# Kernel tuning notes

Measured on AMD Instinct MI355X. Metric: run time of the kernel, lower is better.

Reference implementation:

```python
import jax, jax.numpy as jnp
import numpy as np

N_NODES = 200000
N_SUPER = 20000
N_EDGES = 640000
EMB = 256


def setup_inputs() -> dict:
    key = jax.random.key(0)
    ks = jax.random.split(key, 8)
    x = jax.random.normal(ks[0], (N_NODES, EMB), dtype=jnp.float32)
    new_supernode_x = jax.random.normal(ks[1], (N_SUPER, EMB), dtype=jnp.float32)
    supernode_edge_index = jax.random.randint(ks[2], (2, N_EDGES), 0, N_NODES, dtype=jnp.int64)
    # supernode indices must be unique (torch `x[idx] += v` assumes no duplicate writes)
    supernode_idx = jnp.arange(N_SUPER, dtype=jnp.int64)
    graph_batch = jax.random.randint(ks[3], (N_NODES,), 0, 1024, dtype=jnp.int64)  # unused by forward
    s = 1.0 / np.sqrt(EMB)  # torch.nn.Linear default init scale
    W1 = jax.random.uniform(ks[4], (EMB, EMB), minval=-s, maxval=s, dtype=jnp.float32)
    b1 = jax.random.uniform(ks[5], (EMB,), minval=-s, maxval=s, dtype=jnp.float32)
    W2 = jax.random.uniform(ks[6], (EMB, EMB), minval=-s, maxval=s, dtype=jnp.float32)
    b2 = jax.random.uniform(ks[7], (EMB,), minval=-s, maxval=s, dtype=jnp.float32)
    return {
        "x": x,
        "new_supernode_x": new_supernode_x,
        "supernode_edge_index": supernode_edge_index,
        "supernode_idx": supernode_idx,
        "graph_batch": graph_batch,
        "W1": W1,
        "b1": b1,
        "W2": W2,
        "b2": b2,
    }


def reference(x, new_supernode_x, supernode_edge_index, supernode_idx, graph_batch, W1, b1, W2, b2):
    # step 1: project metagraph supernode embeddings, add into bg-graph rows at supernode_idx
    sn_proj = new_supernode_x @ W1.T + b1                 # [S, D]
    x1 = x.at[supernode_idx].add(sn_proj)                 # [N, D]
    # step 2: gather src rows (AFTER step-1 update), project, scatter-add to dst rows
    src = supernode_edge_index[1]
    dst = supernode_edge_index[0]
    msg = x1[src] @ W2.T + b2                             # [E, D]
    return x1.at[dst].add(msg)                            # [N, D]
```

## Files before the change

kernel.cpp:

```cpp
#include <hip/hip_runtime.h>

#define N_NODES 200000
#define N_SUPER 20000
#define N_EDGES 640000
#define EMB 256

typedef unsigned short ushort_t;
typedef unsigned short ushort8 __attribute__((ext_vector_type(8)));

static __device__ __forceinline__ ushort_t f2bf(float f) {
    unsigned int b = __float_as_uint(f);
    unsigned int r = (b + 0x7FFFu + ((b >> 16) & 1u)) >> 16;
    return (ushort_t)r;
}

__global__ __launch_bounds__(256) void copy_f4(const float4* __restrict__ s,
                                               float4* __restrict__ d, int n) {
    int i = blockIdx.x * 256 + threadIdx.x;
    if (i < n) d[i] = s[i];
}

__global__ __launch_bounds__(256) void hist_dst(const int* __restrict__ ei,
                                                int* __restrict__ counts) {
    int e = blockIdx.x * 256 + threadIdx.x;
    if (e < N_EDGES) atomicAdd(&counts[ei[e]], 1);
}

__global__ __launch_bounds__(256) void block_sums(const int* __restrict__ counts,
                                                  int* __restrict__ partials, int N) {
    __shared__ int sh[256];
    int tid = threadIdx.x;
    int i = blockIdx.x * 256 + tid;
    sh[tid] = (i < N) ? counts[i] : 0;
    __syncthreads();
    for (int off = 128; off > 0; off >>= 1) {
        if (tid < off) sh[tid] += sh[tid + off];
        __syncthreads();
    }
    if (tid == 0) partials[blockIdx.x] = sh[0];
}

__global__ __launch_bounds__(256) void scan_partials(int* __restrict__ partials, int NB) {
    __shared__ int sh[256];
    int tid = threadIdx.x;
    int carry = 0;
    for (int c0 = 0; c0 < NB; c0 += 256) {
        int i = c0 + tid;
        int v = (i < NB) ? partials[i] : 0;
        sh[tid] = v;
        __syncthreads();
        for (int off = 1; off < 256; off <<= 1) {
            int t = (tid >= off) ? sh[tid - off] : 0;
            __syncthreads();
            sh[tid] += t;
            __syncthreads();
        }
        int incl = sh[tid];
        int total = sh[255];
        if (i < NB) partials[i] = carry + incl - v;
        carry += total;
        __syncthreads();
    }
}

__global__ __launch_bounds__(256) void scan_blocks(const int* __restrict__ counts,
                                                   const int* __restrict__ partials,
                                                   int* __restrict__ base, int N) {
    __shared__ int sh[256];
    int tid = threadIdx.x;
    int b = blockIdx.x;
    int i = b * 256 + tid;
    int c = (i < N) ? counts[i] : 0;
    sh[tid] = c;
    __syncthreads();
    for (int off = 1; off < 256; off <<= 1) {
        int t = (tid >= off) ? sh[tid - off] : 0;
        __syncthreads();
        sh[tid] += t;
        __syncthreads();
    }
    if (i < N) base[i] = partials[b] + sh[tid] - c;
    if (i == N - 1) base[N] = partials[b] + sh[tid];
}

__global__ __launch_bounds__(256) void fill_bucket(const int* __restrict__ ei,
                                                   const int* __restrict__ base,
                                                   int* __restrict__ cursor,
                                                   int* __restrict__ bucket) {
    int e = blockIdx.x * 256 + threadIdx.x;
    if (e >= N_EDGES) return;
    int d = ei[e];
    int s = ei[N_EDGES + e];
    int pos = atomicAdd(&cursor[d], 1);
    bucket[base[d] + pos] = s;
}

__global__ __launch_bounds__(256) void gather_sum(const int* __restrict__ bucket,
                                                  const int* __restrict__ base,
                                                  const float* __restrict__ x1,
                                                  ushort_t* __restrict__ agg) {
    int node = blockIdx.x * 4 + (threadIdx.x >> 6);
    int lane = threadIdx.x & 63;
    if (node >= N_NODES) return;
    int j0 = base[node], j1 = base[node + 1];
    float4 acc = make_float4(0.f, 0.f, 0.f, 0.f);
    for (int j = j0; j < j1; ++j) {
        int s = bucket[j];
        float4 v = *(const float4*)(x1 + (size_t)s * EMB + lane * 4);
        acc.x += v.x; acc.y += v.y; acc.z += v.z; acc.w += v.w;
    }
    ushort4 p;
    p.x = f2bf(acc.x); p.y = f2bf(acc.y); p.z = f2bf(acc.z); p.w = f2bf(acc.w);
    *(ushort4*)(agg + (size_t)node * EMB + lane * 4) = p;
}

template <bool A_BF16>
__global__ __launch_bounds__(256) void gemm_add(
    const void* __restrict__ Ap, const float* __restrict__ W,
    const float* __restrict__ bias, const int* __restrict__ deg,
    const int* __restrict__ idx, float* __restrict__ out, int M) {
    __shared__ float At[64][68];
    __shared__ float Wt[64][68];
    const int row0 = blockIdx.x * 64;
    const int col0 = blockIdx.y * 64;
    const int tid = threadIdx.x;
    const int tr = tid >> 4, tc = tid & 15;
    float acc[4][4] = {};

    for (int k0 = 0; k0 < EMB; k0 += 64) {
        __syncthreads();
        if constexpr (A_BF16) {
            const ushort_t* A = (const ushort_t*)Ap;
            for (int t = tid; t < 512; t += 256) {
                int r = t >> 3, kq = t & 7;
                int m = row0 + r;
                float vals[8] = {0, 0, 0, 0, 0, 0, 0, 0};
                if (m < M) {
                    ushort8 u = *(const ushort8*)(A + (size_t)m * EMB + k0 + kq * 8);
                    #pragma unroll
                    for (int j = 0; j < 8; ++j)
                        vals[j] = __uint_as_float((unsigned int)u[j] << 16);
                }
                #pragma unroll
                for (int j = 0; j < 8; ++j) At[kq * 8 + j][r] = vals[j];
            }
        } else {
            const float* A = (const float*)Ap;
            for (int t = tid; t < 1024; t += 256) {
                int r = t >> 4, kq = t & 15;
                int m = row0 + r;
                float4 v = make_float4(0.f, 0.f, 0.f, 0.f);
                if (m < M) v = *(const float4*)(A + (size_t)m * EMB + k0 + kq * 4);
                At[kq * 4 + 0][r] = v.x; At[kq * 4 + 1][r] = v.y;
                At[kq * 4 + 2][r] = v.z; At[kq * 4 + 3][r] = v.w;
            }
        }
        for (int t = tid; t < 1024; t += 256) {
            int r = t >> 4, kq = t & 15;
            float4 w = *(const float4*)(W + (size_t)(col0 + r) * EMB + k0 + kq * 4);
            Wt[kq * 4 + 0][r] = w.x; Wt[kq * 4 + 1][r] = w.y;
            Wt[kq * 4 + 2][r] = w.z; Wt[kq * 4 + 3][r] = w.w;
        }
        __syncthreads();
        #pragma unroll 8
        for (int k = 0; k < 64; ++k) {
            float4 a = *(const float4*)&At[k][tr * 4];
            float4 w = *(const float4*)&Wt[k][tc * 4];
            float av[4] = {a.x, a.y, a.z, a.w};
            float wv[4] = {w.x, w.y, w.z, w.w};
            #pragma unroll
            for (int i = 0; i < 4; ++i)
                #pragma unroll
                for (int j = 0; j < 4; ++j)
                    acc[i][j] += av[i] * wv[j];
        }
    }

    #pragma unroll
    for (int i = 0; i < 4; ++i) {
        int m = row0 + tr * 4 + i;
        if (m >= M) continue;
        int orow = idx ? idx[m] : m;
        float coef = deg ? (float)deg[m] : 1.0f;
        float* op = out + (size_t)orow * EMB + col0 + tc * 4;
        #pragma unroll
        for (int j = 0; j < 4; ++j)
            op[j] += acc[i][j] + bias[col0 + tc * 4 + j] * coef;
    }
}

extern "C" void kernel_launch(void* const* d_in, const int* in_sizes, int n_in,
                              void* d_out, int out_size, void* d_ws, size_t ws_size,
                              hipStream_t stream) {
    const float* x    = (const float*)d_in[0];
    const float* snx  = (const float*)d_in[1];
    const int*   ei   = (const int*)d_in[2];
    const int*   sidx = (const int*)d_in[3];
    const float* W1   = (const float*)d_in[5];
    const float* b1   = (const float*)d_in[6];
    const float* W2   = (const float*)d_in[7];
    const float* b2   = (const float*)d_in[8];
    float* out = (float*)d_out;

    ushort_t* agg  = (ushort_t*)d_ws;
    int* counts    = (int*)(agg + (size_t)N_NODES * EMB);
    int* cursor    = counts + N_NODES;
    int* base      = cursor + N_NODES;
    int* bucket    = base + (N_NODES + 1);
    int* partials  = bucket + N_EDGES;

    const int NB = (N_NODES + 255) / 256;

    hipMemsetAsync(counts, 0, 2 * N_NODES * sizeof(int), stream);

    int n4 = N_NODES * EMB / 4;
    copy_f4<<<(n4 + 255) / 256, 256, 0, stream>>>((const float4*)x, (float4*)out, n4);

    dim3 g1((N_SUPER + 63) / 64, EMB / 64);
    gemm_add<false><<<g1, 256, 0, stream>>>(snx, W1, b1, nullptr, sidx, out, N_SUPER);

    hist_dst<<<(N_EDGES + 255) / 256, 256, 0, stream>>>(ei, counts);
    block_sums<<<NB, 256, 0, stream>>>(counts, partials, N_NODES);
    scan_partials<<<1, 256, 0, stream>>>(partials, NB);
    scan_blocks<<<NB, 256, 0, stream>>>(counts, partials, base, N_NODES);
    fill_bucket<<<(N_EDGES + 255) / 256, 256, 0, stream>>>(ei, base, cursor, bucket);

    gather_sum<<<(N_NODES + 3) / 4, 256, 0, stream>>>(bucket, base, out, agg);

    dim3 g2((N_NODES + 63) / 64, EMB / 64);
    gemm_add<true><<<g2, 256, 0, stream>>>(agg, W2, b2, counts, nullptr, out, N_NODES);
}
```

Baseline: 1.029 ms.

## Replace FP32 SIMT GEMMs with split-bf16 MFMA kernels holding weights in registers

Both projection GEMMs now run on bf16 MFMA instructions instead of scalar FP32 FMAs through shared memory. W is split into high and low bf16 parts so accuracy stays close to FP32, and the FP32 A input is split the same way for the W1 GEMM. Each 512-thread block keeps all of W in registers across a persistent loop over 16-row tiles, so there is no shared-memory staging and no syncthreads. The cost is extra MFMA passes for the split and heavy register use. The tile math also assumes M is a multiple of 16, with no row bounds check.

```diff
diff --git a/kernel.cpp b/kernel.cpp
--- a/kernel.cpp
+++ b/kernel.cpp
@@ -6,7 +6,8 @@
 #define EMB 256
 
 typedef unsigned short ushort_t;
-typedef unsigned short ushort8 __attribute__((ext_vector_type(8)));
+typedef __attribute__((ext_vector_type(8))) short bf16x8;
+typedef __attribute__((ext_vector_type(4))) float f32x4;
 
 static __device__ __forceinline__ ushort_t f2bf(float f) {
     unsigned int b = __float_as_uint(f);
@@ -115,77 +116,91 @@
 }
 
 template <bool A_BF16>
-__global__ __launch_bounds__(256) void gemm_add(
+__global__ __launch_bounds__(512) void gemm_mfma(
     const void* __restrict__ Ap, const float* __restrict__ W,
     const float* __restrict__ bias, const int* __restrict__ deg,
-    const int* __restrict__ idx, float* __restrict__ out, int M) {
-    __shared__ float At[64][68];
-    __shared__ float Wt[64][68];
-    const int row0 = blockIdx.x * 64;
-    const int col0 = blockIdx.y * 64;
-    const int tid = threadIdx.x;
-    const int tr = tid >> 4, tc = tid & 15;
-    float acc[4][4] = {};
-
-    for (int k0 = 0; k0 < EMB; k0 += 64) {
-        __syncthreads();
+    const int* __restrict__ idx, float* __restrict__ out,
+    int M, int ntiles) {
+    const int lane = threadIdx.x & 63;
+    const int wave = threadIdx.x >> 6;
+    const int col0 = wave * 32;
+    const int lcol = lane & 15;
+    const int lk8  = (lane >> 4) * 8;
+
+    bf16x8 bh[2][8], bl[2][8];
+    #pragma unroll
+    for (int nt = 0; nt < 2; ++nt) {
+        const float* wr = W + (size_t)(col0 + nt * 16 + lcol) * EMB + lk8;
+        #pragma unroll
+        for (int kk = 0; kk < 8; ++kk) {
+            float4 u0 = *(const float4*)(wr + kk * 32);
+            float4 u1 = *(const float4*)(wr + kk * 32 + 4);
+            float uv[8] = {u0.x, u0.y, u0.z, u0.w, u1.x, u1.y, u1.z, u1.w};
+            bf16x8 h, l;
+            #pragma unroll
+            for (int j = 0; j < 8; ++j) {
+                ushort_t hb = f2bf(uv[j]);
+                h[j] = (short)hb;
+                float hf = __uint_as_float((unsigned int)hb << 16);
+                l[j] = (short)f2bf(uv[j] - hf);
+            }
+            bh[nt][kk] = h;
+            bl[nt][kk] = l;
+        }
+    }
+    float bias_v[2];
+    #pragma unroll
+    for (int nt = 0; nt < 2; ++nt) bias_v[nt] = bias[col0 + nt * 16 + lcol];
+
+    for (int tile = blockIdx.x; tile < ntiles; tile += gridDim.x) {
+        const int row0 = tile * 16;
+        f32x4 acc[2] = {{0.f, 0.f, 0.f, 0.f}, {0.f, 0.f, 0.f, 0.f}};
+
         if constexpr (A_BF16) {
-            const ushort_t* A = (const ushort_t*)Ap;
-            for (int t = tid; t < 512; t += 256) {
-                int r = t >> 3, kq = t & 7;
-                int m = row0 + r;
-                float vals[8] = {0, 0, 0, 0, 0, 0, 0, 0};
-                if (m < M) {
-                    ushort8 u = *(const ushort8*)(A + (size_t)m * EMB + k0 + kq * 8);
-                    #pragma unroll
-                    for (int j = 0; j < 8; ++j)
-                        vals[j] = __uint_as_float((unsigned int)u[j] << 16);
+            const ushort_t* A0 = (const ushort_t*)Ap + (size_t)(row0 + lcol) * EMB + lk8;
+            #pragma unroll
+            for (int kk = 0; kk < 8; ++kk) {
+                bf16x8 a = *(const bf16x8*)(A0 + kk * 32);
+                #pragma unroll
+                for (int nt = 0; nt < 2; ++nt) {
+                    acc[nt] = __builtin_amdgcn_mfma_f32_16x16x32_bf16(a, bh[nt][kk], acc[nt], 0, 0, 0);
+                    acc[nt] = __builtin_amdgcn_mfma_f32_16x16x32_bf16(a, bl[nt][kk], acc[nt], 0, 0, 0);
+                }
+            }
+        } else {
+            const float* A0 = (const float*)Ap + (size_t)(row0 + lcol) * EMB + lk8;
+            #pragma unroll
+            for (int kk = 0; kk < 8; ++kk) {
+                float4 a0 = *(const float4*)(A0 + kk * 32);
+                float4 a1 = *(const float4*)(A0 + kk * 32 + 4);
+                float av[8] = {a0.x, a0.y, a0.z, a0.w, a1.x, a1.y, a1.z, a1.w};
+                bf16x8 ah, al;
+                #pragma unroll
+                for (int j = 0; j < 8; ++j) {
+                    ushort_t hb = f2bf(av[j]);
+                    ah[j] = (short)hb;
+                    float hf = __uint_as_float((unsigned int)hb << 16);
+                    al[j] = (short)f2bf(av[j] - hf);
                 }
                 #pragma unroll
-                for (int j = 0; j < 8; ++j) At[kq * 8 + j][r] = vals[j];
+                for (int nt = 0; nt < 2; ++nt) {
+                    acc[nt] = __builtin_amdgcn_mfma_f32_16x16x32_bf16(ah, bh[nt][kk], acc[nt], 0, 0, 0);
+                    acc[nt] = __builtin_amdgcn_mfma_f32_16x16x32_bf16(al, bh[nt][kk], acc[nt], 0, 0, 0);
+                    acc[nt] = __builtin_amdgcn_mfma_f32_16x16x32_bf16(ah, bl[nt][kk], acc[nt], 0, 0, 0);
+                }
             }
-        } else {
-            const float* A = (const float*)Ap;
-            for (int t = tid; t < 1024; t += 256) {
-                int r = t >> 4, kq = t & 15;
-                int m = row0 + r;
-                float4 v = make_float4(0.f, 0.f, 0.f, 0.f);
-                if (m < M) v = *(const float4*)(A + (size_t)m * EMB + k0 + kq * 4);
-                At[kq * 4 + 0][r] = v.x; At[kq * 4 + 1][r] = v.y;
-                At[kq * 4 + 2][r] = v.z; At[kq * 4 + 3][r] = v.w;
-            }
-        }
-        for (int t = tid; t < 1024; t += 256) {
-            int r = t >> 4, kq = t & 15;
-            float4 w = *(const float4*)(W + (size_t)(col0 + r) * EMB + k0 + kq * 4);
-            Wt[kq * 4 + 0][r] = w.x; Wt[kq * 4 + 1][r] = w.y;
-            Wt[kq * 4 + 2][r] = w.z; Wt[kq * 4 + 3][r] = w.w;
-        }
-        __syncthreads();
-        #pragma unroll 8
-        for (int k = 0; k < 64; ++k) {
-            float4 a = *(const float4*)&At[k][tr * 4];
-            float4 w = *(const float4*)&Wt[k][tc * 4];
-            float av[4] = {a.x, a.y, a.z, a.w};
-            float wv[4] = {w.x, w.y, w.z, w.w};
-            #pragma unroll
-            for (int i = 0; i < 4; ++i)
-                #pragma unroll
-                for (int j = 0; j < 4; ++j)
-                    acc[i][j] += av[i] * wv[j];
-        }
-    }
-
-    #pragma unroll
-    for (int i = 0; i < 4; ++i) {
-        int m = row0 + tr * 4 + i;
-        if (m >= M) continue;
-        int orow = idx ? idx[m] : m;
-        float coef = deg ? (float)deg[m] : 1.0f;
-        float* op = out + (size_t)orow * EMB + col0 + tc * 4;
+        }
+
         #pragma unroll
-        for (int j = 0; j < 4; ++j)
-            op[j] += acc[i][j] + bias[col0 + tc * 4 + j] * coef;
+        for (int j = 0; j < 4; ++j) {
+            const int r = row0 + (lane >> 4) * 4 + j;
+            const int orow = idx ? idx[r] : r;
+            const float coef = deg ? (float)deg[r] : 1.0f;
+            float* op = out + (size_t)orow * EMB + col0 + lcol;
+            #pragma unroll
+            for (int nt = 0; nt < 2; ++nt)
+                op[nt * 16] += acc[nt][j] + bias_v[nt] * coef;
+        }
     }
 }
 
@@ -216,8 +231,8 @@
     int n4 = N_NODES * EMB / 4;
     copy_f4<<<(n4 + 255) / 256, 256, 0, stream>>>((const float4*)x, (float4*)out, n4);
 
-    dim3 g1((N_SUPER + 63) / 64, EMB / 64);
-    gemm_add<false><<<g1, 256, 0, stream>>>(snx, W1, b1, nullptr, sidx, out, N_SUPER);
+    gemm_mfma<false><<<512, 512, 0, stream>>>(snx, W1, b1, nullptr, sidx, out,
+                                              N_SUPER, N_SUPER / 16);
 
     hist_dst<<<(N_EDGES + 255) / 256, 256, 0, stream>>>(ei, counts);
     block_sums<<<NB, 256, 0, stream>>>(counts, partials, N_NODES);
@@ -227,6 +242,6 @@
 
     gather_sum<<<(N_NODES + 3) / 4, 256, 0, stream>>>(bucket, base, out, agg);
 
-    dim3 g2((N_NODES + 63) / 64, EMB / 64);
-    gemm_add<true><<<g2, 256, 0, stream>>>(agg, W2, b2, counts, nullptr, out, N_NODES);
-}
+    gemm_mfma<true><<<1024, 512, 0, stream>>>(agg, W2, b2, counts, nullptr, out,
+                                              N_NODES, N_NODES / 16);
+}
```

After: 970.1 us. -5.7%, faster.
